# Optimization experiments

Hardware: AMD Instinct MI355X
Metric: run time of the kernel (lower is better)

Reference implementation:

```python
import jax, jax.numpy as jnp
import numpy as np

H = 768        # bert hidden_size
HID = 512      # lstm_hidden
HALF = HID // 2
T = 20         # tagset_size
START, STOP = 18, 19
S = 16386      # input positions incl. CLS/SEP
NEG = -10000.0


def setup_inputs() -> dict:
    key = jax.random.key(0)
    ks = jax.random.split(key, 12)
    sc_x = 1.0
    x = jax.random.normal(ks[0], (1, S, H), dtype=jnp.float32)
    # PyTorch LSTM params (gate order i,f,g,o), one layer, bidirectional
    s_ih = 1.0 / np.sqrt(HALF)
    w_ih_f = jax.random.uniform(ks[1], (4 * HALF, H), jnp.float32, -s_ih, s_ih)
    w_hh_f = jax.random.uniform(ks[2], (4 * HALF, HALF), jnp.float32, -s_ih, s_ih)
    b_ih_f = jax.random.uniform(ks[3], (4 * HALF,), jnp.float32, -s_ih, s_ih)
    b_hh_f = jax.random.uniform(ks[4], (4 * HALF,), jnp.float32, -s_ih, s_ih)
    w_ih_b = jax.random.uniform(ks[5], (4 * HALF, H), jnp.float32, -s_ih, s_ih)
    w_hh_b = jax.random.uniform(ks[6], (4 * HALF, HALF), jnp.float32, -s_ih, s_ih)
    b_ih_b = jax.random.uniform(ks[7], (4 * HALF,), jnp.float32, -s_ih, s_ih)
    b_hh_b = jax.random.uniform(ks[8], (4 * HALF,), jnp.float32, -s_ih, s_ih)
    s_t = 1.0 / np.sqrt(HID)
    w_tag = jax.random.uniform(ks[9], (T, HID), jnp.float32, -s_t, s_t)
    b_tag = jax.random.uniform(ks[10], (T,), jnp.float32, -s_t, s_t)
    transitions = jax.random.normal(ks[11], (T, T), dtype=jnp.float32)
    transitions = transitions.at[START, :].set(NEG).at[:, STOP].set(NEG)
    return {
        "x": x,
        "w_ih_f": w_ih_f, "w_hh_f": w_hh_f, "b_ih_f": b_ih_f, "b_hh_f": b_hh_f,
        "w_ih_b": w_ih_b, "w_hh_b": w_hh_b, "b_ih_b": b_ih_b, "b_hh_b": b_hh_b,
        "w_tag": w_tag, "b_tag": b_tag, "transitions": transitions,
    }


def _lstm_one_step(xt, w_ih, b_ih, b_hh):
    # Original passes [1, N, H] to a batch_first=False LSTM => seq_len=1,
    # batch=N, zero initial state. So each token does ONE cell step:
    # h0=c0=0 => hh contribution is only b_hh.
    g = xt @ w_ih.T + b_ih + b_hh          # [N, 4*HALF]
    i, f, gg, o = jnp.split(g, 4, axis=-1)  # PyTorch gate order i,f,g,o
    c = jax.nn.sigmoid(i) * jnp.tanh(gg)    # f*c0 = 0
    return jax.nn.sigmoid(o) * jnp.tanh(c)  # [N, HALF]


def reference(x, w_ih_f, w_hh_f, b_ih_f, b_hh_f,
              w_ih_b, w_hh_b, b_ih_b, b_hh_b,
              w_tag, b_tag, transitions):
    tok = x[0, 1:-1, :]                     # narrow(1,1,S-2): drop CLS/SEP -> [N,H]
    h_f = _lstm_one_step(tok, w_ih_f, b_ih_f, b_hh_f)
    h_b = _lstm_one_step(tok, w_ih_b, b_ih_b, b_hh_b)
    enc = jnp.concatenate([h_f, h_b], axis=-1)   # [N, HID]
    feats = enc @ w_tag.T + b_tag                # [N, T] emission scores

    # ---- Viterbi decode (sequential DP over tokens) ----
    init = jnp.full((T,), NEG, dtype=feats.dtype).at[START].set(0.0)

    def vstep(fv, feat):
        scores = fv[None, :] + transitions       # [next_tag, prev_tag]
        bp = jnp.argmax(scores, axis=1)          # backpointers [T]
        fv_new = jnp.max(scores, axis=1) + feat
        return fv_new, bp

    fv, bps = jax.lax.scan(vstep, init, feats)   # bps: [N, T]
    terminal = fv + transitions[STOP]
    best = jnp.argmax(terminal)
    path_score = terminal[best]

    def btrack(b, bp):
        return bp[b], b                          # emit tag at time t, move to t-1

    _, best_path = jax.lax.scan(btrack, best, bps, reverse=True)  # [N] in time order
    return path_score, best_path
```

## Files before the change

### kernel.cpp

```cpp
#include <hip/hip_runtime.h>
#include <math.h>

#define HDIM 768
#define HIDD 512
#define NTOK 16384
#define NT 20
#define CHUNKS 128
#define CLEN 128

typedef unsigned short ushort_t;
typedef __attribute__((ext_vector_type(8))) short bf16x8;
typedef __attribute__((ext_vector_type(4))) float f32x4;

__device__ __forceinline__ float sigm(float x){ return 1.0f/(1.0f+expf(-x)); }

__device__ __forceinline__ ushort_t f2bf(float f){
    unsigned int u = __float_as_uint(f);
    unsigned int r = (u + 0x7fffu + ((u >> 16) & 1u)) >> 16;
    return (ushort_t)r;
}
__device__ __forceinline__ float bf2f(ushort_t b){
    return __uint_as_float(((unsigned int)b) << 16);
}

#define GLD16(gp, lp) __builtin_amdgcn_global_load_lds( \
    (const __attribute__((address_space(1))) void*)(gp), \
    (__attribute__((address_space(3))) void*)(lp), 16, 0, 0)

__global__ __launch_bounds__(256) void conv_kernel(
    const float* __restrict__ x,
    const float* __restrict__ wf, const float* __restrict__ wb,
    ushort_t* __restrict__ Ah, ushort_t* __restrict__ Al,
    ushort_t* __restrict__ Bh, ushort_t* __restrict__ Bl)
{
    const int bid = blockIdx.x;
    if (bid < 1152){
        int t = bid*256 + threadIdx.x;
        int n = t / 192, c4 = (t - n*192)*4;
        int dir = n / 768, nr = n - dir*768;
        int gate = nr >> 8, j = nr & 255;
        int wrow = j + ((gate==0)?0:((gate==1)?512:768));
        const float* src = dir ? wb : wf;
        const float4 v = *(const float4*)(src + (size_t)wrow*HDIM + c4);
        float f[4] = {v.x, v.y, v.z, v.w};
        ushort_t h[4], l[4];
        #pragma unroll
        for (int i=0;i<4;++i){
            h[i] = f2bf(f[i]);
            l[i] = f2bf(f[i] - bf2f(h[i]));
        }
        *(ushort4*)(Bh + (size_t)n*HDIM + c4) = make_ushort4(h[0],h[1],h[2],h[3]);
        *(ushort4*)(Bl + (size_t)n*HDIM + c4) = make_ushort4(l[0],l[1],l[2],l[3]);
    } else {
        int t = (bid-1152)*256 + threadIdx.x;
        int row = t / 192, c4 = (t - row*192)*4;
        const float4 v = *(const float4*)(x + (size_t)(row+1)*HDIM + c4);
        float f[4] = {v.x, v.y, v.z, v.w};
        ushort_t h[4], l[4];
        #pragma unroll
        for (int i=0;i<4;++i){
            h[i] = f2bf(f[i]);
            l[i] = f2bf(f[i] - bf2f(h[i]));
        }
        *(ushort4*)(Ah + (size_t)row*HDIM + c4) = make_ushort4(h[0],h[1],h[2],h[3]);
        *(ushort4*)(Al + (size_t)row*HDIM + c4) = make_ushort4(l[0],l[1],l[2],l[3]);
    }
}

__global__ __launch_bounds__(256, 2) void gemm_fused(
    const ushort_t* __restrict__ Ah, const ushort_t* __restrict__ Al,
    const ushort_t* __restrict__ Bh, const ushort_t* __restrict__ Bl,
    const float* __restrict__ bihf, const float* __restrict__ bhhf,
    const float* __restrict__ bihb, const float* __restrict__ bhhb,
    const float* __restrict__ wtag, float* __restrict__ featsp)
{
    __shared__ __align__(16) char smem[65536];
    ushort_t* As_h = (ushort_t*)smem;
    ushort_t* As_l = (ushort_t*)(smem + 16384);
    ushort_t* Bs_h = (ushort_t*)(smem + 32768);
    ushort_t* Bs_l = (ushort_t*)(smem + 49152);
    float* hbuf = (float*)smem;
    float* wts  = (float*)(smem + 33024);

    const int tid = threadIdx.x;
    const int bx = blockIdx.x;
    const int bm = bx >> 2, q = bx & 3;
    const int dir = q >> 1, j0 = (q & 1)*128;
    const int row0 = bm*128;
    const float* __restrict__ bih = dir ? bihb : bihf;
    const float* __restrict__ bhh = dir ? bhhb : bhhf;

    const int lane = tid & 63, wv = tid >> 6;
    const int wm = wv >> 1, wn = wv & 1;
    const int lm = lane & 15, lq = lane >> 4;
    const int wbase = (tid & 192) * 8;

    const int smr = tid >> 3;
    const int k8x = (tid & 7) ^ (smr & 7);
    size_t aoff[4];
    #pragma unroll
    for (int g=0; g<4; ++g)
        aoff[g] = (size_t)(row0 + g*32 + smr)*HDIM + k8x*8;

    int jcol[4];
    #pragma unroll
    for (int fn=0; fn<4; ++fn) jcol[fn] = j0 + wn*64 + fn*16 + lm;

    float held[4][4][4];
    f32x4 acc[4][4];

    #pragma unroll 1
    for (int p=0; p<3; ++p){
        const int nbase = dir*768 + p*256 + j0;
        size_t boff[4];
        #pragma unroll
        for (int g=0; g<4; ++g)
            boff[g] = (size_t)(nbase + g*32 + smr)*HDIM + k8x*8;

        #pragma unroll
        for (int fm=0; fm<4; ++fm)
            #pragma unroll
            for (int fn=0; fn<4; ++fn)
                acc[fm][fn] = (f32x4){0.f,0.f,0.f,0.f};

        #pragma unroll 1
        for (int kt=0; kt<12; ++kt){
            const int k0 = kt*64;
            #pragma unroll
            for (int g=0; g<4; ++g){
                GLD16(Ah + aoff[g] + k0, &As_h[g*2048 + wbase]);
                GLD16(Al + aoff[g] + k0, &As_l[g*2048 + wbase]);
                GLD16(Bh + boff[g] + k0, &Bs_h[g*2048 + wbase]);
                GLD16(Bl + boff[g] + k0, &Bs_l[g*2048 + wbase]);
            }
            __syncthreads();
            #pragma unroll
            for (int kc=0; kc<2; ++kc){
                bf16x8 afh[4], afl[4], bfh[4], bfl[4];
                #pragma unroll
                for (int f=0; f<4; ++f){
                    int m = wm*64 + f*16 + lm;
                    int sa = (m*8 + ((kc*4+lq) ^ (m&7)))*8;
                    afh[f] = *(const bf16x8*)&As_h[sa];
                    afl[f] = *(const bf16x8*)&As_l[sa];
                    int n = wn*64 + f*16 + lm;
                    int sb = (n*8 + ((kc*4+lq) ^ (n&7)))*8;
                    bfh[f] = *(const bf16x8*)&Bs_h[sb];
                    bfl[f] = *(const bf16x8*)&Bs_l[sb];
                }
                #pragma unroll
                for (int fm=0; fm<4; ++fm)
                    #pragma unroll
                    for (int fn=0; fn<4; ++fn){
                        acc[fm][fn] = __builtin_amdgcn_mfma_f32_16x16x32_bf16(
                            afh[fm], bfh[fn], acc[fm][fn], 0, 0, 0);
                        acc[fm][fn] = __builtin_amdgcn_mfma_f32_16x16x32_bf16(
                            afl[fm], bfh[fn], acc[fm][fn], 0, 0, 0);
                        acc[fm][fn] = __builtin_amdgcn_mfma_f32_16x16x32_bf16(
                            afh[fm], bfl[fn], acc[fm][fn], 0, 0, 0);
                    }
            }
            __syncthreads();
        }

        const int gbase = (p==0) ? 0 : ((p==1) ? 512 : 768);
        float bias[4];
        #pragma unroll
        for (int fn=0; fn<4; ++fn)
            bias[fn] = bih[gbase + jcol[fn]] + bhh[gbase + jcol[fn]];

        if (p==0){
            #pragma unroll
            for (int fm=0; fm<4; ++fm)
                #pragma unroll
                for (int fn=0; fn<4; ++fn)
                    #pragma unroll
                    for (int r=0; r<4; ++r)
                        held[fm][fn][r] = sigm(acc[fm][fn][r] + bias[fn]);
        } else if (p==1){
            #pragma unroll
            for (int fm=0; fm<4; ++fm)
                #pragma unroll
                for (int fn=0; fn<4; ++fn)
                    #pragma unroll
                    for (int r=0; r<4; ++r)
                        held[fm][fn][r] *= tanhf(acc[fm][fn][r] + bias[fn]);
        } else {
            float hv[4][4][4];
            #pragma unroll
            for (int fm=0; fm<4; ++fm)
                #pragma unroll
                for (int fn=0; fn<4; ++fn)
                    #pragma unroll
                    for (int r=0; r<4; ++r)
                        hv[fm][fn][r] = sigm(acc[fm][fn][r] + bias[fn]) * tanhf(held[fm][fn][r]);

            for (int idx=tid; idx<NT*128; idx+=256){
                int t = idx >> 7, j = idx & 127;
                wts[idx] = wtag[t*HIDD + dir*256 + j0 + j];
            }
            float* fq = featsp + (size_t)q * (NTOK*NT);
            #pragma unroll 1
            for (int ph=0; ph<2; ++ph){
                __syncthreads();
                if (wm == ph){
                    #pragma unroll
                    for (int fm=0; fm<4; ++fm)
                        #pragma unroll
                        for (int fn=0; fn<4; ++fn)
                            #pragma unroll
                            for (int r=0; r<4; ++r){
                                int mloc = fm*16 + lq*4 + r;
                                int jloc = wn*64 + fn*16 + lm;
                                hbuf[mloc*129 + jloc] = hv[fm][fn][r];
                            }
                }
                __syncthreads();
                const int mrow = tid & 63, tg0 = (tid >> 6) * 5;
                float s[5] = {0.f,0.f,0.f,0.f,0.f};
                for (int j=0;j<128;++j){
                    float h = hbuf[mrow*129 + j];
                    #pragma unroll
                    for (int tt=0; tt<5; ++tt)
                        s[tt] = fmaf(h, wts[(tg0+tt)*128 + j], s[tt]);
                }
                const int mglob = row0 + ph*64 + mrow;
                #pragma unroll
                for (int tt=0; tt<5; ++tt)
                    fq[(size_t)mglob*NT + tg0 + tt] = s[tt];
            }
        }
    }
}

__device__ __forceinline__ void load_fl(
    const float* __restrict__ featsp, const float* __restrict__ btg,
    float* fl, int c, int tid, int nthr)
{
    const float4* p0 = (const float4*)(featsp);
    const float4* p1 = (const float4*)(featsp + (size_t)NTOK*NT);
    const float4* p2 = (const float4*)(featsp + (size_t)2*NTOK*NT);
    const float4* p3 = (const float4*)(featsp + (size_t)3*NTOK*NT);
    const int base = c*(CLEN*NT/4);
    for (int idx=tid; idx<CLEN*NT/4; idx+=nthr){
        float4 a = p0[base+idx], b = p1[base+idx];
        float4 d = p2[base+idx], e = p3[base+idx];
        float4 v;
        v.x = (a.x+b.x)+(d.x+e.x);
        v.y = (a.y+b.y)+(d.y+e.y);
        v.z = (a.z+b.z)+(d.z+e.z);
        v.w = (a.w+b.w)+(d.w+e.w);
        int t0 = (idx*4) % 20;
        v.x += btg[t0]; v.y += btg[t0+1]; v.z += btg[t0+2]; v.w += btg[t0+3];
        ((float4*)fl)[idx] = v;
    }
}

__global__ __launch_bounds__(512) void vit_chunkmat(
    const float* __restrict__ featsp, const float* __restrict__ btag,
    const float* __restrict__ trans, float* __restrict__ Pall)
{
    __shared__ float fl[CLEN*NT];
    __shared__ float Pb[2][NT*NT];
    const int c = blockIdx.x, tid = threadIdx.x;
    load_fl(featsp, btag, fl, c, tid, 512);
    const bool act = tid < NT*NT;
    const int i = tid/20, j = tid - i*20;
    float tr[NT];
    if (act){
        #pragma unroll
        for (int k=0;k<NT;++k) tr[k] = trans[i*NT+k];
        Pb[0][tid] = (i==j) ? 0.f : -1e30f;
    }
    __syncthreads();
    int cur = 0;
    for (int t=0;t<CLEN;++t){
        float m = -3.0e38f;
        if (act){
            #pragma unroll
            for (int k=0;k<NT;++k) m = fmaxf(m, tr[k] + Pb[cur][k*NT+j]);
            m += fl[t*NT+i];
            Pb[cur^1][tid] = m;
        }
        __syncthreads();
        cur ^= 1;
    }
    if (act) Pall[(size_t)c*(NT*NT) + tid] = Pb[cur][tid];
}

__global__ __launch_bounds__(128) void vit_scan(
    const float* __restrict__ Pall, const float* __restrict__ trans,
    float* __restrict__ fvstart, float* __restrict__ dout, int* __restrict__ bestws)
{
    __shared__ float Pb[NT*NT];
    __shared__ float fv[NT];
    const int tid = threadIdx.x;
    float4 pn = {0.f,0.f,0.f,0.f};
    if (tid<100) pn = ((const float4*)Pall)[tid];
    if (tid<NT) fv[tid] = (tid==18) ? 0.f : -10000.f;
    for (int c=0;c<CHUNKS;++c){
        if (tid<100) ((float4*)Pb)[tid] = pn;
        if (tid<100 && c+1<CHUNKS) pn = ((const float4*)(Pall + (size_t)(c+1)*(NT*NT)))[tid];
        __syncthreads();
        if (tid<NT) fvstart[c*NT+tid] = fv[tid];
        float nf = -3.0e38f;
        if (tid<NT){
            #pragma unroll
            for (int j=0;j<NT;++j) nf = fmaxf(nf, Pb[tid*NT+j] + fv[j]);
        }
        __syncthreads();
        if (tid<NT) fv[tid] = nf;
    }
    __syncthreads();
    if (tid==0){
        float best = -3.0e38f; int bidx = 0;
        for (int j=0;j<NT;++j){
            float tv = fv[j] + trans[19*NT+j];
            if (tv > best){ best = tv; bidx = j; }
        }
        dout[0] = best;
        bestws[0] = bidx;
    }
}

__global__ __launch_bounds__(64) void vit_replay(
    const float* __restrict__ featsp, const float* __restrict__ btag,
    const float* __restrict__ trans, const float* __restrict__ fvstart,
    unsigned int* __restrict__ bpout, int* __restrict__ Hout)
{
    __shared__ float fl[CLEN*NT];
    __shared__ float fv[NT];
    __shared__ unsigned char bp[CLEN*NT];
    const int c = blockIdx.x, tid = threadIdx.x;
    load_fl(featsp, btag, fl, c, tid, 64);
    float tr[NT];
    if (tid<NT){
        fv[tid] = fvstart[c*NT+tid];
        #pragma unroll
        for (int k=0;k<NT;++k) tr[k] = trans[tid*NT+k];
    }
    __syncthreads();
    for (int t=0;t<CLEN;++t){
        float best = 0.f; int bj = 0;
        if (tid<NT){
            best = tr[0] + fv[0];
            #pragma unroll
            for (int j=1;j<NT;++j){
                float v = tr[j] + fv[j];
                if (v > best){ best = v; bj = j; }
            }
        }
        __syncthreads();
        if (tid<NT){
            fv[tid] = best + fl[t*NT+tid];
            bp[t*NT+tid] = (unsigned char)bj;
        }
        __syncthreads();
    }
    for (int idx=tid; idx<CLEN*NT/4; idx+=64)
        bpout[(size_t)c*(CLEN*NT/4) + idx] = ((unsigned int*)bp)[idx];
    if (tid<NT){
        int m = tid;
        for (int t=CLEN-1;t>=0;--t) m = bp[t*NT+m];
        Hout[c*NT+tid] = m;
    }
}

__global__ __launch_bounds__(64) void bt_fill(
    const unsigned int* __restrict__ bpin, const int* __restrict__ Hin,
    const int* __restrict__ bestws, float* __restrict__ dout)
{
    __shared__ int Hl[CHUNKS*NT];
    __shared__ unsigned char bp[CLEN*NT];
    __shared__ float ob[CLEN];
    const int c = blockIdx.x, tid = threadIdx.x;
    for (int idx=tid; idx<CHUNKS*NT; idx+=64) Hl[idx] = Hin[idx];
    for (int idx=tid; idx<CLEN*NT/4; idx+=64)
        ((unsigned int*)bp)[idx] = bpin[(size_t)c*(CLEN*NT/4) + idx];
    __syncthreads();
    if (tid==0){
        int e = bestws[0];
        for (int cc=CHUNKS-1; cc>c; --cc) e = Hl[cc*NT+e];
        for (int t=CLEN-1;t>=0;--t){ ob[t] = (float)e; e = bp[t*NT+e]; }
    }
    __syncthreads();
    for (int idx=tid; idx<CLEN; idx+=64)
        dout[1 + c*CLEN + idx] = ob[idx];
}

extern "C" void kernel_launch(void* const* d_in, const int* in_sizes, int n_in,
                              void* d_out, int out_size, void* d_ws, size_t ws_size,
                              hipStream_t stream)
{
    const float* x    = (const float*)d_in[0];
    const float* wf   = (const float*)d_in[1];
    const float* bihf = (const float*)d_in[3];
    const float* bhhf = (const float*)d_in[4];
    const float* wb   = (const float*)d_in[5];
    const float* bihb = (const float*)d_in[7];
    const float* bhhb = (const float*)d_in[8];
    const float* wtag = (const float*)d_in[9];
    const float* btag = (const float*)d_in[10];
    const float* trans= (const float*)d_in[11];
    float* out = (float*)d_out;

    char* w = (char*)d_ws;
    ushort_t* Ah = (ushort_t*)w;         w += 25165824;
    ushort_t* Al = (ushort_t*)w;         w += 25165824;
    ushort_t* Bh = (ushort_t*)w;         w += 2359296;
    ushort_t* Bl = (ushort_t*)w;         w += 2359296;
    float* featsp = (float*)w;           w += 5242880;
    float* Pall  = (float*)w;            w += 204800;
    float* fvst  = (float*)w;            w += 10240;
    int* Hmap    = (int*)w;              w += 10240;
    unsigned int* bp = (unsigned int*)w; w += 327680;
    int* best    = (int*)w;

    conv_kernel<<<13440, 256, 0, stream>>>(x, wf, wb, Ah, Al, Bh, Bl);
    gemm_fused<<<512, 256, 0, stream>>>(Ah, Al, Bh, Bl, bihf, bhhf, bihb, bhhb,
                                        wtag, featsp);
    vit_chunkmat<<<CHUNKS, 512, 0, stream>>>(featsp, btag, trans, Pall);
    vit_scan<<<1, 128, 0, stream>>>(Pall, trans, fvst, out, best);
    vit_replay<<<CHUNKS, 64, 0, stream>>>(featsp, btag, trans, fvst, bp, Hmap);
    bt_fill<<<CHUNKS, 64, 0, stream>>>(bp, Hmap, best, out);
}
```

Before: 440.3 us.

## Halve GEMM M-tile and K-step to raise occupancy and add XCD-aware block mapping

The fused LSTM GEMM now uses a 64-row M tile and a 32-wide K step, which halves shared memory to 32KB and the accumulator registers. Launch bounds go to 4 blocks per CU and the grid doubles to 1024 blocks. Block indices are remapped so consecutive M tiles are spread across the 8 XCDs, and the LDS swizzle and tag-projection epilogue are adjusted for the smaller tile. The aim is more resident waves and better load balance across CUs, at the cost of lower per-block reuse of the B tiles, twice as many barriers per K, and 3/8 of the threads idle in the epilogue.

```diff
diff --git a/kernel.cpp b/kernel.cpp
--- a/kernel.cpp
+++ b/kernel.cpp
@@ -67,26 +67,27 @@
     }
 }
 
-__global__ __launch_bounds__(256, 2) void gemm_fused(
+__global__ __launch_bounds__(256, 4) void gemm_fused(
     const ushort_t* __restrict__ Ah, const ushort_t* __restrict__ Al,
     const ushort_t* __restrict__ Bh, const ushort_t* __restrict__ Bl,
     const float* __restrict__ bihf, const float* __restrict__ bhhf,
     const float* __restrict__ bihb, const float* __restrict__ bhhb,
     const float* __restrict__ wtag, float* __restrict__ featsp)
 {
-    __shared__ __align__(16) char smem[65536];
+    __shared__ __align__(16) char smem[32768];
     ushort_t* As_h = (ushort_t*)smem;
-    ushort_t* As_l = (ushort_t*)(smem + 16384);
-    ushort_t* Bs_h = (ushort_t*)(smem + 32768);
-    ushort_t* Bs_l = (ushort_t*)(smem + 49152);
+    ushort_t* As_l = (ushort_t*)(smem + 4096);
+    ushort_t* Bs_h = (ushort_t*)(smem + 8192);
+    ushort_t* Bs_l = (ushort_t*)(smem + 16384);
     float* hbuf = (float*)smem;
-    float* wts  = (float*)(smem + 33024);
+    float* wts  = (float*)(smem + 16512);
 
     const int tid = threadIdx.x;
     const int bx = blockIdx.x;
-    const int bm = bx >> 2, q = bx & 3;
+    const int xcd = bx & 7, bidx = bx >> 3;
+    const int q = bidx & 3, mt = (bidx >> 2)*8 + xcd;
     const int dir = q >> 1, j0 = (q & 1)*128;
-    const int row0 = bm*128;
+    const int row0 = mt*64;
     const float* __restrict__ bih = dir ? bihb : bihf;
     const float* __restrict__ bhh = dir ? bhhb : bhhf;
 
@@ -95,71 +96,77 @@
     const int lm = lane & 15, lq = lane >> 4;
     const int wbase = (tid & 192) * 8;
 
-    const int smr = tid >> 3;
-    const int k8x = (tid & 7) ^ (smr & 7);
-    size_t aoff[4];
+    const int sr = tid >> 2;
+    const int k8s = (tid & 3) ^ ((sr & 3) ^ ((sr >> 2) & 3));
+    const size_t aoffe = (size_t)(row0 + sr)*HDIM + k8s*8;
+    size_t boffe[2];
     #pragma unroll
-    for (int g=0; g<4; ++g)
-        aoff[g] = (size_t)(row0 + g*32 + smr)*HDIM + k8x*8;
+    for (int g=0; g<2; ++g)
+        boffe[g] = (size_t)(g*64 + sr)*HDIM + k8s*8;
+
+    int aoff_lds[2], boff_lds[4];
+    #pragma unroll
+    for (int f=0; f<2; ++f){
+        int m = wm*32 + f*16 + lm;
+        int k8p = (lq ^ (m & 3) ^ ((m >> 2) & 3)) & 3;
+        aoff_lds[f] = (m*4 + k8p)*8;
+    }
+    #pragma unroll
+    for (int f=0; f<4; ++f){
+        int n = wn*64 + f*16 + lm;
+        int k8p = (lq ^ (n & 3) ^ ((n >> 2) & 3)) & 3;
+        boff_lds[f] = (n*4 + k8p)*8;
+    }
 
     int jcol[4];
     #pragma unroll
     for (int fn=0; fn<4; ++fn) jcol[fn] = j0 + wn*64 + fn*16 + lm;
 
-    float held[4][4][4];
-    f32x4 acc[4][4];
+    float held[2][4][4];
+    f32x4 acc[2][4];
 
     #pragma unroll 1
     for (int p=0; p<3; ++p){
-        const int nbase = dir*768 + p*256 + j0;
-        size_t boff[4];
-        #pragma unroll
-        for (int g=0; g<4; ++g)
-            boff[g] = (size_t)(nbase + g*32 + smr)*HDIM + k8x*8;
-
-        #pragma unroll
-        for (int fm=0; fm<4; ++fm)
+        const size_t bbase = (size_t)(dir*768 + p*256 + j0)*HDIM;
+
+        #pragma unroll
+        for (int fm=0; fm<2; ++fm)
             #pragma unroll
             for (int fn=0; fn<4; ++fn)
                 acc[fm][fn] = (f32x4){0.f,0.f,0.f,0.f};
 
         #pragma unroll 1
-        for (int kt=0; kt<12; ++kt){
-            const int k0 = kt*64;
-            #pragma unroll
-            for (int g=0; g<4; ++g){
-                GLD16(Ah + aoff[g] + k0, &As_h[g*2048 + wbase]);
-                GLD16(Al + aoff[g] + k0, &As_l[g*2048 + wbase]);
-                GLD16(Bh + boff[g] + k0, &Bs_h[g*2048 + wbase]);
-                GLD16(Bl + boff[g] + k0, &Bs_l[g*2048 + wbase]);
+        for (int kt=0; kt<24; ++kt){
+            const int k0 = kt*32;
+            GLD16(Ah + aoffe + k0,            &As_h[wbase]);
+            GLD16(Al + aoffe + k0,            &As_l[wbase]);
+            GLD16(Bh + bbase + boffe[0] + k0, &Bs_h[wbase]);
+            GLD16(Bh + bbase + boffe[1] + k0, &Bs_h[2048 + wbase]);
+            GLD16(Bl + bbase + boffe[0] + k0, &Bs_l[wbase]);
+            GLD16(Bl + bbase + boffe[1] + k0, &Bs_l[2048 + wbase]);
+            __syncthreads();
+            bf16x8 afh[2], afl[2], bfh[4], bfl[4];
+            #pragma unroll
+            for (int f=0; f<2; ++f){
+                afh[f] = *(const bf16x8*)&As_h[aoff_lds[f]];
+                afl[f] = *(const bf16x8*)&As_l[aoff_lds[f]];
             }
-            __syncthreads();
-            #pragma unroll
-            for (int kc=0; kc<2; ++kc){
-                bf16x8 afh[4], afl[4], bfh[4], bfl[4];
+            #pragma unroll
+            for (int f=0; f<4; ++f){
+                bfh[f] = *(const bf16x8*)&Bs_h[boff_lds[f]];
+                bfl[f] = *(const bf16x8*)&Bs_l[boff_lds[f]];
+            }
+            #pragma unroll
+            for (int fm=0; fm<2; ++fm)
                 #pragma unroll
-                for (int f=0; f<4; ++f){
-                    int m = wm*64 + f*16 + lm;
-                    int sa = (m*8 + ((kc*4+lq) ^ (m&7)))*8;
-                    afh[f] = *(const bf16x8*)&As_h[sa];
-                    afl[f] = *(const bf16x8*)&As_l[sa];
-                    int n = wn*64 + f*16 + lm;
-                    int sb = (n*8 + ((kc*4+lq) ^ (n&7)))*8;
-                    bfh[f] = *(const bf16x8*)&Bs_h[sb];
-                    bfl[f] = *(const bf16x8*)&Bs_l[sb];
+                for (int fn=0; fn<4; ++fn){
+                    acc[fm][fn] = __builtin_amdgcn_mfma_f32_16x16x32_bf16(
+                        afh[fm], bfh[fn], acc[fm][fn], 0, 0, 0);
+                    acc[fm][fn] = __builtin_amdgcn_mfma_f32_16x16x32_bf16(
+                        afl[fm], bfh[fn], acc[fm][fn], 0, 0, 0);
+                    acc[fm][fn] = __builtin_amdgcn_mfma_f32_16x16x32_bf16(
+                        afh[fm], bfl[fn], acc[fm][fn], 0, 0, 0);
                 }
-                #pragma unroll
-                for (int fm=0; fm<4; ++fm)
-                    #pragma unroll
-                    for (int fn=0; fn<4; ++fn){
-                        acc[fm][fn] = __builtin_amdgcn_mfma_f32_16x16x32_bf16(
-                            afh[fm], bfh[fn], acc[fm][fn], 0, 0, 0);
-                        acc[fm][fn] = __builtin_amdgcn_mfma_f32_16x16x32_bf16(
-                            afl[fm], bfh[fn], acc[fm][fn], 0, 0, 0);
-                        acc[fm][fn] = __builtin_amdgcn_mfma_f32_16x16x32_bf16(
-                            afh[fm], bfl[fn], acc[fm][fn], 0, 0, 0);
-                    }
-            }
             __syncthreads();
         }
 
@@ -171,7 +178,7 @@
 
         if (p==0){
             #pragma unroll
-            for (int fm=0; fm<4; ++fm)
+            for (int fm=0; fm<2; ++fm)
                 #pragma unroll
                 for (int fn=0; fn<4; ++fn)
                     #pragma unroll
@@ -179,25 +186,25 @@
                         held[fm][fn][r] = sigm(acc[fm][fn][r] + bias[fn]);
         } else if (p==1){
             #pragma unroll
-            for (int fm=0; fm<4; ++fm)
+            for (int fm=0; fm<2; ++fm)
                 #pragma unroll
                 for (int fn=0; fn<4; ++fn)
                     #pragma unroll
                     for (int r=0; r<4; ++r)
                         held[fm][fn][r] *= tanhf(acc[fm][fn][r] + bias[fn]);
         } else {
-            float hv[4][4][4];
-            #pragma unroll
-            for (int fm=0; fm<4; ++fm)
+            float hv[2][4][4];
+            #pragma unroll
+            for (int fm=0; fm<2; ++fm)
                 #pragma unroll
                 for (int fn=0; fn<4; ++fn)
                     #pragma unroll
                     for (int r=0; r<4; ++r)
                         hv[fm][fn][r] = sigm(acc[fm][fn][r] + bias[fn]) * tanhf(held[fm][fn][r]);
 
-            for (int idx=tid; idx<NT*128; idx+=256){
-                int t = idx >> 7, j = idx & 127;
-                wts[idx] = wtag[t*HIDD + dir*256 + j0 + j];
+            for (int i2=tid; i2<NT*128; i2+=256){
+                int t = i2 >> 7, j = i2 & 127;
+                wts[i2] = wtag[t*HIDD + dir*256 + j0 + j];
             }
             float* fq = featsp + (size_t)q * (NTOK*NT);
             #pragma unroll 1
@@ -205,7 +212,7 @@
                 __syncthreads();
                 if (wm == ph){
                     #pragma unroll
-                    for (int fm=0; fm<4; ++fm)
+                    for (int fm=0; fm<2; ++fm)
                         #pragma unroll
                         for (int fn=0; fn<4; ++fn)
                             #pragma unroll
@@ -216,18 +223,21 @@
                             }
                 }
                 __syncthreads();
-                const int mrow = tid & 63, tg0 = (tid >> 6) * 5;
-                float s[5] = {0.f,0.f,0.f,0.f,0.f};
-                for (int j=0;j<128;++j){
-                    float h = hbuf[mrow*129 + j];
+                const int mrow = tid & 31, grp = tid >> 5;
+                if (grp < 5){
+                    const int tg0 = grp*4;
+                    float s[4] = {0.f,0.f,0.f,0.f};
+                    for (int j=0;j<128;++j){
+                        float h = hbuf[mrow*129 + j];
+                        #pragma unroll
+                        for (int tt=0; tt<4; ++tt)
+                            s[tt] = fmaf(h, wts[(tg0+tt)*128 + j], s[tt]);
+                    }
+                    const int mglob = row0 + ph*32 + mrow;
                     #pragma unroll
-                    for (int tt=0; tt<5; ++tt)
-                        s[tt] = fmaf(h, wts[(tg0+tt)*128 + j], s[tt]);
+                    for (int tt=0; tt<4; ++tt)
+                        fq[(size_t)mglob*NT + tg0 + tt] = s[tt];
                 }
-                const int mglob = row0 + ph*64 + mrow;
-                #pragma unroll
-                for (int tt=0; tt<5; ++tt)
-                    fq[(size_t)mglob*NT + tg0 + tt] = s[tt];
             }
         }
     }
@@ -417,8 +427,8 @@
     int* best    = (int*)w;
 
     conv_kernel<<<13440, 256, 0, stream>>>(x, wf, wb, Ah, Al, Bh, Bl);
-    gemm_fused<<<512, 256, 0, stream>>>(Ah, Al, Bh, Bl, bihf, bhhf, bihb, bhhb,
-                                        wtag, featsp);
+    gemm_fused<<<1024, 256, 0, stream>>>(Ah, Al, Bh, Bl, bihf, bhhf, bihb, bhhb,
+                                         wtag, featsp);
     vit_chunkmat<<<CHUNKS, 512, 0, stream>>>(featsp, btag, trans, Pall);
     vit_scan<<<1, 128, 0, stream>>>(Pall, trans, fvst, out, best);
     vit_replay<<<CHUNKS, 64, 0, stream>>>(featsp, btag, trans, fvst, bp, Hmap);
```

Measured after the change: 446.2 us. About the same (+1.3%).
